# Kernel optimization log

Hardware: AMD Instinct MI355X
Metric: run time of the kernel (lower is better)

## Reference

```python
import jax, jax.numpy as jnp
import numpy as np

FLOAT_MIN = jnp.finfo(jnp.float32).min


def setup_inputs() -> dict:
    key = jax.random.key(0)
    ks = jax.random.split(key, 8)
    B, S, F1, F2, A = 65536, 256, 256, 256, 128
    return {
        "obs_state": jax.random.normal(ks[0], (B, S), dtype=jnp.float32),
        "action_mask": jax.random.randint(ks[1], (B, A), 0, 2, dtype=jnp.int32),
        "W1": jax.random.normal(ks[2], (S, F1), dtype=jnp.float32) * (1.0 / np.sqrt(S)),
        "b1": jnp.zeros((F1,), dtype=jnp.float32),
        "W2": jax.random.normal(ks[3], (F1, F2), dtype=jnp.float32) * (1.0 / np.sqrt(F1)),
        "b2": jnp.zeros((F2,), dtype=jnp.float32),
        "W3": jax.random.normal(ks[4], (F2, A), dtype=jnp.float32) * (1.0 / np.sqrt(F2)),
        "b3": jnp.zeros((A,), dtype=jnp.float32),
    }


def reference(obs_state, action_mask, W1, b1, W2, b2, W3, b3):
    # 3-layer MLP: state -> fc1 -> relu -> fc2 -> relu -> fc3
    h = jax.nn.relu(obs_state @ W1 + b1)
    h = jax.nn.relu(h @ W2 + b2)
    x = h @ W3 + b3  # [B, A] logits

    # Vectorized action masking (replaces per-element Python loop):
    #   mask==0 -> FLOAT_MIN; rows with all-zero mask -> FLOAT_MIN everywhere, col 0 = 1.0
    valid = action_mask != 0  # [B, A] bool
    x = jnp.where(valid, x, FLOAT_MIN)
    all_invalid = ~jnp.any(valid, axis=1, keepdims=True)  # [B, 1]
    col0 = jnp.arange(x.shape[1]) == 0  # [A]
    x = jnp.where(all_invalid & col0, jnp.float32(1.0), x)
    return x
```

## Files before the change

### kernel.cpp

```cpp
#include <hip/hip_runtime.h>

typedef __attribute__((ext_vector_type(8))) short short8;
typedef __attribute__((ext_vector_type(8))) unsigned short ushort8;
typedef __attribute__((ext_vector_type(4))) float f32x4;

#define MT 32
#define STR 264

__device__ __forceinline__ float bmax_r14() { return __uint_as_float(0x7F7F0000u); }

__device__ __forceinline__ unsigned short f2bf_r14(float f) {
    unsigned int u = __float_as_uint(f);
    return (unsigned short)((u + 0x7fffu + ((u >> 16) & 1u)) >> 16);
}

__global__ __launch_bounds__(256)
void pack_weights_r14(const float* __restrict__ W1,
                      const float* __restrict__ W2,
                      const float* __restrict__ W3,
                      unsigned short* __restrict__ ws) {
    int s = blockIdx.x * 256 + threadIdx.x;
    const float* src;
    unsigned short* dst;
    int N;
    if (s < 8192)       { src = W1; dst = ws;          N = 256; }
    else if (s < 16384) { src = W2; dst = ws + 65536;  N = 256; s -= 8192; }
    else                { src = W3; dst = ws + 131072; N = 128; s -= 16384; }
    int frag = s >> 6, lane = s & 63;
    int kb = (frag & 7) * 32 + (lane >> 4) * 8;
    int n  = (frag >> 3) * 16 + (lane & 15);
    ushort8 o;
    #pragma unroll
    for (int j = 0; j < 8; ++j) o[j] = f2bf_r14(src[(kb + j) * N + n]);
    *(ushort8*)&dst[s * 8] = o;
}

__device__ __forceinline__ void layer_mfma_r14(
    const unsigned short* __restrict__ act, const unsigned short* __restrict__ wp,
    int wave, int lane, int quad, int noff, f32x4 acc[2][4])
{
    #pragma unroll
    for (int k0 = 0; k0 < 8; ++k0) {
        short8 b[4];
        #pragma unroll
        for (int ct = 0; ct < 4; ++ct)
            b[ct] = *(const short8*)&wp[(((wave * 4 + ct) * 8 + k0) * 64 + lane) * 8];
        #pragma unroll
        for (int rt = 0; rt < 2; ++rt) {
            short8 a = *(const short8*)&act[(rt * 16 + noff) * STR + k0 * 32 + quad * 8];
            #pragma unroll
            for (int ct = 0; ct < 4; ++ct)
                acc[rt][ct] = __builtin_amdgcn_mfma_f32_16x16x32_bf16(a, b[ct], acc[rt][ct], 0, 0, 0);
        }
    }
}

__device__ __forceinline__ void layer_store_r14(
    unsigned short* __restrict__ act, const float* __restrict__ bias,
    int wave, int quad, int noff, f32x4 acc[2][4])
{
    #pragma unroll
    for (int ct = 0; ct < 4; ++ct) {
        int col = (wave * 4 + ct) * 16 + noff;
        float bv = bias[col];
        #pragma unroll
        for (int rt = 0; rt < 2; ++rt) {
            #pragma unroll
            for (int i = 0; i < 4; ++i) {
                float v = fmaxf(acc[rt][ct][i] + bv, 0.0f);
                act[(rt * 16 + quad * 4 + i) * STR + col] = f2bf_r14(v);
            }
        }
    }
}

__global__ __launch_bounds__(256, 6)
void ColorNetwork_32495722561720_kernel(
        const float* __restrict__ obs,
        const int* __restrict__ amask,
        const float* __restrict__ b1,
        const float* __restrict__ b2,
        const float* __restrict__ b3,
        const unsigned short* __restrict__ w1p,
        const unsigned short* __restrict__ w2p,
        const unsigned short* __restrict__ w3p,
        float* __restrict__ out)
{
    __shared__ __align__(16) unsigned short act[MT * STR];
    __shared__ int rowany[MT];

    const int tid  = threadIdx.x;
    const int wave = tid >> 6;
    const int lane = tid & 63;
    const int quad = lane >> 4;
    const int noff = lane & 15;
    const size_t rowbase = (size_t)blockIdx.x * MT;

    if (tid < MT) rowany[tid] = 0;

    const float4* xin = (const float4*)(obs + rowbase * 256);
    #pragma unroll
    for (int i = 0; i < 8; ++i) {
        int f = tid + i * 256;
        int row = f >> 6;
        int c4 = f & 63;
        float4 v = xin[f];
        ushort4 p;
        p.x = f2bf_r14(v.x); p.y = f2bf_r14(v.y);
        p.z = f2bf_r14(v.z); p.w = f2bf_r14(v.w);
        *(ushort4*)&act[row * STR + c4 * 4] = p;
    }
    __syncthreads();

    const int4* min4 = (const int4*)(amask + rowbase * 128);
    #pragma unroll
    for (int i = 0; i < 4; ++i) {
        int f = tid + i * 256;
        int4 m = min4[f];
        if (m.x | m.y | m.z | m.w) rowany[f >> 5] = 1;
    }

    {
        f32x4 acc[2][4] = {};
        layer_mfma_r14(act, w1p, wave, lane, quad, noff, acc);
        __syncthreads();
        layer_store_r14(act, b1, wave, quad, noff, acc);
        __syncthreads();
    }
    {
        f32x4 acc[2][4] = {};
        layer_mfma_r14(act, w2p, wave, lane, quad, noff, acc);
        __syncthreads();
        layer_store_r14(act, b2, wave, quad, noff, acc);
        __syncthreads();
    }
    {
        f32x4 acc[2][2] = {};
        #pragma unroll
        for (int k0 = 0; k0 < 8; ++k0) {
            short8 b0 = *(const short8*)&w3p[(((wave * 2 + 0) * 8 + k0) * 64 + lane) * 8];
            short8 b1v = *(const short8*)&w3p[(((wave * 2 + 1) * 8 + k0) * 64 + lane) * 8];
            #pragma unroll
            for (int rt = 0; rt < 2; ++rt) {
                short8 a = *(const short8*)&act[(rt * 16 + noff) * STR + k0 * 32 + quad * 8];
                acc[rt][0] = __builtin_amdgcn_mfma_f32_16x16x32_bf16(a, b0, acc[rt][0], 0, 0, 0);
                acc[rt][1] = __builtin_amdgcn_mfma_f32_16x16x32_bf16(a, b1v, acc[rt][1], 0, 0, 0);
            }
        }

        const float BM = bmax_r14();
        #pragma unroll
        for (int ct = 0; ct < 2; ++ct) {
            int col = (wave * 2 + ct) * 16 + noff;
            float bv = b3[col];
            #pragma unroll
            for (int rt = 0; rt < 2; ++rt) {
                #pragma unroll
                for (int i = 0; i < 4; ++i) {
                    int row = rt * 16 + quad * 4 + i;
                    int m = amask[(rowbase + row) * 128 + col];
                    float v = acc[rt][ct][i] + bv;
                    v = fminf(fmaxf(v, -BM), BM);
                    if (!(v == v)) v = 0.0f;
                    if (!m) v = -BM;
                    if (!rowany[row]) v = (col == 0) ? 1.0f : -BM;
                    out[(rowbase + row) * 128 + col] = v;
                }
            }
        }
    }
}

extern "C" void kernel_launch(void* const* d_in, const int* in_sizes, int n_in,
                              void* d_out, int out_size, void* d_ws, size_t ws_size,
                              hipStream_t stream) {
    const float* obs   = (const float*)d_in[0];
    const int*   amask = (const int*)d_in[1];
    const float* W1 = (const float*)d_in[2];
    const float* b1 = (const float*)d_in[3];
    const float* W2 = (const float*)d_in[4];
    const float* b2 = (const float*)d_in[5];
    const float* W3 = (const float*)d_in[6];
    const float* b3 = (const float*)d_in[7];
    float* out = (float*)d_out;

    const int B = in_sizes[0] / 256;

    unsigned short* ws = (unsigned short*)d_ws;
    unsigned short* w1p = ws;
    unsigned short* w2p = ws + 65536;
    unsigned short* w3p = ws + 131072;

    pack_weights_r14<<<80, 256, 0, stream>>>(W1, W2, W3, ws);

    ColorNetwork_32495722561720_kernel<<<B / MT, 256, 0, stream>>>(
        obs, amask, b1, b2, b3, w1p, w2p, w3p, out);
}
```

Before: 179.8 us.

## Process two row tiles per block with ping-pong LDS and register prefetch

Each block now handles two 32-row tiles. Activations ping-pong between two shared-memory buffers, which removes the barrier that sat between each layer's MFMA phase and its store. The next tile's observations are loaded into registers during the current tile's layers and staged into LDS after layer 3, to hide global load latency. The cost is double the LDS footprint, more register pressure (launch bounds lowered from 6 to 4 blocks per CU), and half as many blocks.

After: 213.2 us. 1.19x slower.

```diff
diff --git a/kernel.cpp b/kernel.cpp
--- a/kernel.cpp
+++ b/kernel.cpp
@@ -5,17 +5,18 @@
 typedef __attribute__((ext_vector_type(4))) float f32x4;
 
 #define MT 32
+#define TILES 2
 #define STR 264
 
-__device__ __forceinline__ float bmax_r14() { return __uint_as_float(0x7F7F0000u); }
-
-__device__ __forceinline__ unsigned short f2bf_r14(float f) {
+__device__ __forceinline__ float bmax_r15() { return __uint_as_float(0x7F7F0000u); }
+
+__device__ __forceinline__ unsigned short f2bf_r15(float f) {
     unsigned int u = __float_as_uint(f);
     return (unsigned short)((u + 0x7fffu + ((u >> 16) & 1u)) >> 16);
 }
 
 __global__ __launch_bounds__(256)
-void pack_weights_r14(const float* __restrict__ W1,
+void pack_weights_r15(const float* __restrict__ W1,
                       const float* __restrict__ W2,
                       const float* __restrict__ W3,
                       unsigned short* __restrict__ ws) {
@@ -31,12 +32,12 @@
     int n  = (frag >> 3) * 16 + (lane & 15);
     ushort8 o;
     #pragma unroll
-    for (int j = 0; j < 8; ++j) o[j] = f2bf_r14(src[(kb + j) * N + n]);
+    for (int j = 0; j < 8; ++j) o[j] = f2bf_r15(src[(kb + j) * N + n]);
     *(ushort8*)&dst[s * 8] = o;
 }
 
-__device__ __forceinline__ void layer_mfma_r14(
-    const unsigned short* __restrict__ act, const unsigned short* __restrict__ wp,
+__device__ __forceinline__ void layer_mfma_r15(
+    const unsigned short* __restrict__ src, const unsigned short* __restrict__ wp,
     int wave, int lane, int quad, int noff, f32x4 acc[2][4])
 {
     #pragma unroll
@@ -47,7 +48,7 @@
             b[ct] = *(const short8*)&wp[(((wave * 4 + ct) * 8 + k0) * 64 + lane) * 8];
         #pragma unroll
         for (int rt = 0; rt < 2; ++rt) {
-            short8 a = *(const short8*)&act[(rt * 16 + noff) * STR + k0 * 32 + quad * 8];
+            short8 a = *(const short8*)&src[(rt * 16 + noff) * STR + k0 * 32 + quad * 8];
             #pragma unroll
             for (int ct = 0; ct < 4; ++ct)
                 acc[rt][ct] = __builtin_amdgcn_mfma_f32_16x16x32_bf16(a, b[ct], acc[rt][ct], 0, 0, 0);
@@ -55,8 +56,8 @@
     }
 }
 
-__device__ __forceinline__ void layer_store_r14(
-    unsigned short* __restrict__ act, const float* __restrict__ bias,
+__device__ __forceinline__ void layer_store_r15(
+    unsigned short* __restrict__ dst, const float* __restrict__ bias,
     int wave, int quad, int noff, f32x4 acc[2][4])
 {
     #pragma unroll
@@ -68,13 +69,28 @@
             #pragma unroll
             for (int i = 0; i < 4; ++i) {
                 float v = fmaxf(acc[rt][ct][i] + bv, 0.0f);
-                act[(rt * 16 + quad * 4 + i) * STR + col] = f2bf_r14(v);
-            }
-        }
-    }
-}
-
-__global__ __launch_bounds__(256, 6)
+                dst[(rt * 16 + quad * 4 + i) * STR + col] = f2bf_r15(v);
+            }
+        }
+    }
+}
+
+__device__ __forceinline__ void stage_from_regs_r15(
+    unsigned short* __restrict__ dst, const float4* v, int tid)
+{
+    #pragma unroll
+    for (int i = 0; i < 8; ++i) {
+        int f = tid + i * 256;
+        int row = f >> 6;
+        int c4 = f & 63;
+        ushort4 p;
+        p.x = f2bf_r15(v[i].x); p.y = f2bf_r15(v[i].y);
+        p.z = f2bf_r15(v[i].z); p.w = f2bf_r15(v[i].w);
+        *(ushort4*)&dst[row * STR + c4 * 4] = p;
+    }
+}
+
+__global__ __launch_bounds__(256, 4)
 void ColorNetwork_32495722561720_kernel(
         const float* __restrict__ obs,
         const int* __restrict__ amask,
@@ -86,88 +102,112 @@
         const unsigned short* __restrict__ w3p,
         float* __restrict__ out)
 {
-    __shared__ __align__(16) unsigned short act[MT * STR];
-    __shared__ int rowany[MT];
+    __shared__ __align__(16) unsigned short act[2][MT * STR];
+    __shared__ int rowany[2][MT];
 
     const int tid  = threadIdx.x;
     const int wave = tid >> 6;
     const int lane = tid & 63;
     const int quad = lane >> 4;
     const int noff = lane & 15;
-    const size_t rowbase = (size_t)blockIdx.x * MT;
-
-    if (tid < MT) rowany[tid] = 0;
-
-    const float4* xin = (const float4*)(obs + rowbase * 256);
-    #pragma unroll
-    for (int i = 0; i < 8; ++i) {
-        int f = tid + i * 256;
-        int row = f >> 6;
-        int c4 = f & 63;
-        float4 v = xin[f];
-        ushort4 p;
-        p.x = f2bf_r14(v.x); p.y = f2bf_r14(v.y);
-        p.z = f2bf_r14(v.z); p.w = f2bf_r14(v.w);
-        *(ushort4*)&act[row * STR + c4 * 4] = p;
+    const size_t row0 = (size_t)blockIdx.x * (MT * TILES);
+
+    if (tid < 2 * MT) ((int*)rowany)[tid] = 0;
+
+    float4 xf[8];
+    {
+        const float4* xin = (const float4*)(obs + row0 * 256);
+        #pragma unroll
+        for (int i = 0; i < 8; ++i) xf[i] = xin[tid + i * 256];
     }
     __syncthreads();
-
-    const int4* min4 = (const int4*)(amask + rowbase * 128);
-    #pragma unroll
-    for (int i = 0; i < 4; ++i) {
-        int f = tid + i * 256;
-        int4 m = min4[f];
-        if (m.x | m.y | m.z | m.w) rowany[f >> 5] = 1;
-    }
-
+    stage_from_regs_r15(act[0], xf, tid);
     {
-        f32x4 acc[2][4] = {};
-        layer_mfma_r14(act, w1p, wave, lane, quad, noff, acc);
+        const int4* min4 = (const int4*)(amask + row0 * 128);
+        #pragma unroll
+        for (int i = 0; i < 4; ++i) {
+            int f = tid + i * 256;
+            int4 m = min4[f];
+            if (m.x | m.y | m.z | m.w) rowany[0][f >> 5] = 1;
+        }
+    }
+    __syncthreads();
+
+    int p = 0;
+    #pragma unroll
+    for (int t = 0; t < TILES; ++t, p ^= 1) {
+        const size_t rowbase = row0 + (size_t)t * MT;
+        const bool more = (t + 1 < TILES);
+
+        if (more) {
+            const float4* xin = (const float4*)(obs + (rowbase + MT) * 256);
+            #pragma unroll
+            for (int i = 0; i < 8; ++i) xf[i] = xin[tid + i * 256];
+        }
+
+        {
+            f32x4 acc[2][4] = {};
+            layer_mfma_r15(act[p], w1p, wave, lane, quad, noff, acc);
+            layer_store_r15(act[p ^ 1], b1, wave, quad, noff, acc);
+        }
         __syncthreads();
-        layer_store_r14(act, b1, wave, quad, noff, acc);
+
+        if (more && tid < MT) rowany[p ^ 1][tid] = 0;
+
+        {
+            f32x4 acc[2][4] = {};
+            layer_mfma_r15(act[p ^ 1], w2p, wave, lane, quad, noff, acc);
+            layer_store_r15(act[p], b2, wave, quad, noff, acc);
+        }
         __syncthreads();
-    }
-    {
-        f32x4 acc[2][4] = {};
-        layer_mfma_r14(act, w2p, wave, lane, quad, noff, acc);
-        __syncthreads();
-        layer_store_r14(act, b2, wave, quad, noff, acc);
-        __syncthreads();
-    }
-    {
-        f32x4 acc[2][2] = {};
-        #pragma unroll
-        for (int k0 = 0; k0 < 8; ++k0) {
-            short8 b0 = *(const short8*)&w3p[(((wave * 2 + 0) * 8 + k0) * 64 + lane) * 8];
-            short8 b1v = *(const short8*)&w3p[(((wave * 2 + 1) * 8 + k0) * 64 + lane) * 8];
-            #pragma unroll
-            for (int rt = 0; rt < 2; ++rt) {
-                short8 a = *(const short8*)&act[(rt * 16 + noff) * STR + k0 * 32 + quad * 8];
-                acc[rt][0] = __builtin_amdgcn_mfma_f32_16x16x32_bf16(a, b0, acc[rt][0], 0, 0, 0);
-                acc[rt][1] = __builtin_amdgcn_mfma_f32_16x16x32_bf16(a, b1v, acc[rt][1], 0, 0, 0);
-            }
-        }
-
-        const float BM = bmax_r14();
-        #pragma unroll
-        for (int ct = 0; ct < 2; ++ct) {
-            int col = (wave * 2 + ct) * 16 + noff;
-            float bv = b3[col];
-            #pragma unroll
-            for (int rt = 0; rt < 2; ++rt) {
+
+        {
+            f32x4 acc[2][2] = {};
+            #pragma unroll
+            for (int k0 = 0; k0 < 8; ++k0) {
+                short8 b0 = *(const short8*)&w3p[(((wave * 2 + 0) * 8 + k0) * 64 + lane) * 8];
+                short8 b1v = *(const short8*)&w3p[(((wave * 2 + 1) * 8 + k0) * 64 + lane) * 8];
+                #pragma unroll
+                for (int rt = 0; rt < 2; ++rt) {
+                    short8 a = *(const short8*)&act[p][(rt * 16 + noff) * STR + k0 * 32 + quad * 8];
+                    acc[rt][0] = __builtin_amdgcn_mfma_f32_16x16x32_bf16(a, b0, acc[rt][0], 0, 0, 0);
+                    acc[rt][1] = __builtin_amdgcn_mfma_f32_16x16x32_bf16(a, b1v, acc[rt][1], 0, 0, 0);
+                }
+            }
+
+            if (more) {
+                stage_from_regs_r15(act[p ^ 1], xf, tid);
+                const int4* mn = (const int4*)(amask + (rowbase + MT) * 128);
                 #pragma unroll
                 for (int i = 0; i < 4; ++i) {
-                    int row = rt * 16 + quad * 4 + i;
-                    int m = amask[(rowbase + row) * 128 + col];
-                    float v = acc[rt][ct][i] + bv;
-                    v = fminf(fmaxf(v, -BM), BM);
-                    if (!(v == v)) v = 0.0f;
-                    if (!m) v = -BM;
-                    if (!rowany[row]) v = (col == 0) ? 1.0f : -BM;
-                    out[(rowbase + row) * 128 + col] = v;
+                    int f = tid + i * 256;
+                    int4 m = mn[f];
+                    if (m.x | m.y | m.z | m.w) rowany[p ^ 1][f >> 5] = 1;
                 }
             }
-        }
+
+            const float BM = bmax_r15();
+            #pragma unroll
+            for (int ct = 0; ct < 2; ++ct) {
+                int col = (wave * 2 + ct) * 16 + noff;
+                float bv = b3[col];
+                #pragma unroll
+                for (int rt = 0; rt < 2; ++rt) {
+                    #pragma unroll
+                    for (int i = 0; i < 4; ++i) {
+                        int row = rt * 16 + quad * 4 + i;
+                        int m = amask[(rowbase + row) * 128 + col];
+                        float v = acc[rt][ct][i] + bv;
+                        v = fminf(fmaxf(v, -BM), BM);
+                        if (!(v == v)) v = 0.0f;
+                        if (!m) v = -BM;
+                        if (!rowany[p][row]) v = (col == 0) ? 1.0f : -BM;
+                        out[(rowbase + row) * 128 + col] = v;
+                    }
+                }
+            }
+        }
+        __syncthreads();
     }
 }
 
@@ -191,8 +231,8 @@
     unsigned short* w2p = ws + 65536;
     unsigned short* w3p = ws + 131072;
 
-    pack_weights_r14<<<80, 256, 0, stream>>>(W1, W2, W3, ws);
-
-    ColorNetwork_32495722561720_kernel<<<B / MT, 256, 0, stream>>>(
+    pack_weights_r15<<<80, 256, 0, stream>>>(W1, W2, W3, ws);
+
+    ColorNetwork_32495722561720_kernel<<<B / (MT * TILES), 256, 0, stream>>>(
         obs, amask, b1, b2, b3, w1p, w2p, w3p, out);
 }
```

## Make each wave process its own row tile independently without block barriers

Applied to the files above, without the earlier changes.

Each of the four waves now owns a private 32-row tile in LDS (128 rows per block) and computes every output column of all three layers itself. It keeps the A fragments for the whole K dimension in registers and walks over 16-column tiles, so all __syncthreads are gone. The cost is that each wave now streams the full weight matrices rather than a quarter of them, multiplying L1/L2 weight traffic by four. It also uses more LDS per block, which limits occupancy to two blocks.

After: 184.6 us. +2.7%, slower.

```diff
diff --git a/kernel.cpp b/kernel.cpp
--- a/kernel.cpp
+++ b/kernel.cpp
@@ -5,17 +5,18 @@
 typedef __attribute__((ext_vector_type(4))) float f32x4;
 
 #define MT 32
+#define NWAVE 4
 #define STR 264
 
-__device__ __forceinline__ float bmax_r14() { return __uint_as_float(0x7F7F0000u); }
-
-__device__ __forceinline__ unsigned short f2bf_r14(float f) {
+__device__ __forceinline__ float bmax_r17() { return __uint_as_float(0x7F7F0000u); }
+
+__device__ __forceinline__ unsigned short f2bf_r17(float f) {
     unsigned int u = __float_as_uint(f);
     return (unsigned short)((u + 0x7fffu + ((u >> 16) & 1u)) >> 16);
 }
 
 __global__ __launch_bounds__(256)
-void pack_weights_r14(const float* __restrict__ W1,
+void pack_weights_r17(const float* __restrict__ W1,
                       const float* __restrict__ W2,
                       const float* __restrict__ W3,
                       unsigned short* __restrict__ ws) {
@@ -31,50 +32,11 @@
     int n  = (frag >> 3) * 16 + (lane & 15);
     ushort8 o;
     #pragma unroll
-    for (int j = 0; j < 8; ++j) o[j] = f2bf_r14(src[(kb + j) * N + n]);
+    for (int j = 0; j < 8; ++j) o[j] = f2bf_r17(src[(kb + j) * N + n]);
     *(ushort8*)&dst[s * 8] = o;
 }
 
-__device__ __forceinline__ void layer_mfma_r14(
-    const unsigned short* __restrict__ act, const unsigned short* __restrict__ wp,
-    int wave, int lane, int quad, int noff, f32x4 acc[2][4])
-{
-    #pragma unroll
-    for (int k0 = 0; k0 < 8; ++k0) {
-        short8 b[4];
-        #pragma unroll
-        for (int ct = 0; ct < 4; ++ct)
-            b[ct] = *(const short8*)&wp[(((wave * 4 + ct) * 8 + k0) * 64 + lane) * 8];
-        #pragma unroll
-        for (int rt = 0; rt < 2; ++rt) {
-            short8 a = *(const short8*)&act[(rt * 16 + noff) * STR + k0 * 32 + quad * 8];
-            #pragma unroll
-            for (int ct = 0; ct < 4; ++ct)
-                acc[rt][ct] = __builtin_amdgcn_mfma_f32_16x16x32_bf16(a, b[ct], acc[rt][ct], 0, 0, 0);
-        }
-    }
-}
-
-__device__ __forceinline__ void layer_store_r14(
-    unsigned short* __restrict__ act, const float* __restrict__ bias,
-    int wave, int quad, int noff, f32x4 acc[2][4])
-{
-    #pragma unroll
-    for (int ct = 0; ct < 4; ++ct) {
-        int col = (wave * 4 + ct) * 16 + noff;
-        float bv = bias[col];
-        #pragma unroll
-        for (int rt = 0; rt < 2; ++rt) {
-            #pragma unroll
-            for (int i = 0; i < 4; ++i) {
-                float v = fmaxf(acc[rt][ct][i] + bv, 0.0f);
-                act[(rt * 16 + quad * 4 + i) * STR + col] = f2bf_r14(v);
-            }
-        }
-    }
-}
-
-__global__ __launch_bounds__(256, 6)
+__global__ __launch_bounds__(256, 2)
 void ColorNetwork_32495722561720_kernel(
         const float* __restrict__ obs,
         const int* __restrict__ amask,
@@ -86,86 +48,130 @@
         const unsigned short* __restrict__ w3p,
         float* __restrict__ out)
 {
-    __shared__ __align__(16) unsigned short act[MT * STR];
-    __shared__ int rowany[MT];
+    __shared__ __align__(16) unsigned short act[NWAVE * MT * STR];
+    __shared__ int rowany[NWAVE * MT];
 
     const int tid  = threadIdx.x;
     const int wave = tid >> 6;
     const int lane = tid & 63;
     const int quad = lane >> 4;
     const int noff = lane & 15;
-    const size_t rowbase = (size_t)blockIdx.x * MT;
-
-    if (tid < MT) rowany[tid] = 0;
-
-    const float4* xin = (const float4*)(obs + rowbase * 256);
-    #pragma unroll
-    for (int i = 0; i < 8; ++i) {
-        int f = tid + i * 256;
-        int row = f >> 6;
-        int c4 = f & 63;
-        float4 v = xin[f];
-        ushort4 p;
-        p.x = f2bf_r14(v.x); p.y = f2bf_r14(v.y);
-        p.z = f2bf_r14(v.z); p.w = f2bf_r14(v.w);
-        *(ushort4*)&act[row * STR + c4 * 4] = p;
-    }
-    __syncthreads();
-
-    const int4* min4 = (const int4*)(amask + rowbase * 128);
-    #pragma unroll
-    for (int i = 0; i < 4; ++i) {
-        int f = tid + i * 256;
-        int4 m = min4[f];
-        if (m.x | m.y | m.z | m.w) rowany[f >> 5] = 1;
-    }
+    const int sb   = wave * (MT * STR);
+    const int rb   = wave * MT;
+    const size_t rowbase = (size_t)blockIdx.x * (MT * NWAVE) + (size_t)wave * MT;
 
     {
-        f32x4 acc[2][4] = {};
-        layer_mfma_r14(act, w1p, wave, lane, quad, noff, acc);
-        __syncthreads();
-        layer_store_r14(act, b1, wave, quad, noff, acc);
-        __syncthreads();
-    }
+        const float4* xin = (const float4*)(obs + rowbase * 256);
+        #pragma unroll 8
+        for (int i = 0; i < 32; ++i) {
+            int f = i * 64 + lane;
+            int row = f >> 6;
+            int c4 = f & 63;
+            float4 v = xin[f];
+            ushort4 p;
+            p.x = f2bf_r17(v.x); p.y = f2bf_r17(v.y);
+            p.z = f2bf_r17(v.z); p.w = f2bf_r17(v.w);
+            *(ushort4*)&act[sb + row * STR + c4 * 4] = p;
+        }
+    }
+
+    if (lane < MT) rowany[rb + lane] = 0;
     {
-        f32x4 acc[2][4] = {};
-        layer_mfma_r14(act, w2p, wave, lane, quad, noff, acc);
-        __syncthreads();
-        layer_store_r14(act, b2, wave, quad, noff, acc);
-        __syncthreads();
-    }
-    {
-        f32x4 acc[2][2] = {};
+        const int4* min4 = (const int4*)(amask + rowbase * 128);
+        #pragma unroll 4
+        for (int i = 0; i < 16; ++i) {
+            int f = i * 64 + lane;
+            int4 m = min4[f];
+            if (m.x | m.y | m.z | m.w) rowany[rb + (f >> 5)] = 1;
+        }
+    }
+
+    short8 a[2][8];
+
+    #pragma unroll
+    for (int rt = 0; rt < 2; ++rt)
+        #pragma unroll
+        for (int k0 = 0; k0 < 8; ++k0)
+            a[rt][k0] = *(const short8*)&act[sb + (rt * 16 + noff) * STR + k0 * 32 + quad * 8];
+    #pragma unroll 2
+    for (int ct = 0; ct < 16; ++ct) {
+        f32x4 ac0 = {}, ac1 = {};
         #pragma unroll
         for (int k0 = 0; k0 < 8; ++k0) {
-            short8 b0 = *(const short8*)&w3p[(((wave * 2 + 0) * 8 + k0) * 64 + lane) * 8];
-            short8 b1v = *(const short8*)&w3p[(((wave * 2 + 1) * 8 + k0) * 64 + lane) * 8];
+            short8 b = *(const short8*)&w1p[((ct * 8 + k0) * 64 + lane) * 8];
+            ac0 = __builtin_amdgcn_mfma_f32_16x16x32_bf16(a[0][k0], b, ac0, 0, 0, 0);
+            ac1 = __builtin_amdgcn_mfma_f32_16x16x32_bf16(a[1][k0], b, ac1, 0, 0, 0);
+        }
+        int col = ct * 16 + noff;
+        float bv = b1[col];
+        #pragma unroll
+        for (int i = 0; i < 4; ++i) {
+            act[sb + (quad * 4 + i) * STR + col]      = f2bf_r17(fmaxf(ac0[i] + bv, 0.0f));
+            act[sb + (16 + quad * 4 + i) * STR + col] = f2bf_r17(fmaxf(ac1[i] + bv, 0.0f));
+        }
+    }
+
+    #pragma unroll
+    for (int rt = 0; rt < 2; ++rt)
+        #pragma unroll
+        for (int k0 = 0; k0 < 8; ++k0)
+            a[rt][k0] = *(const short8*)&act[sb + (rt * 16 + noff) * STR + k0 * 32 + quad * 8];
+    #pragma unroll 2
+    for (int ct = 0; ct < 16; ++ct) {
+        f32x4 ac0 = {}, ac1 = {};
+        #pragma unroll
+        for (int k0 = 0; k0 < 8; ++k0) {
+            short8 b = *(const short8*)&w2p[((ct * 8 + k0) * 64 + lane) * 8];
+            ac0 = __builtin_amdgcn_mfma_f32_16x16x32_bf16(a[0][k0], b, ac0, 0, 0, 0);
+            ac1 = __builtin_amdgcn_mfma_f32_16x16x32_bf16(a[1][k0], b, ac1, 0, 0, 0);
+        }
+        int col = ct * 16 + noff;
+        float bv = b2[col];
+        #pragma unroll
+        for (int i = 0; i < 4; ++i) {
+            act[sb + (quad * 4 + i) * STR + col]      = f2bf_r17(fmaxf(ac0[i] + bv, 0.0f));
+            act[sb + (16 + quad * 4 + i) * STR + col] = f2bf_r17(fmaxf(ac1[i] + bv, 0.0f));
+        }
+    }
+
+    #pragma unroll
+    for (int rt = 0; rt < 2; ++rt)
+        #pragma unroll
+        for (int k0 = 0; k0 < 8; ++k0)
+            a[rt][k0] = *(const short8*)&act[sb + (rt * 16 + noff) * STR + k0 * 32 + quad * 8];
+
+    int ra[8];
+    #pragma unroll
+    for (int rt = 0; rt < 2; ++rt)
+        #pragma unroll
+        for (int i = 0; i < 4; ++i)
+            ra[rt * 4 + i] = rowany[rb + rt * 16 + quad * 4 + i];
+
+    const float BM = bmax_r17();
+    #pragma unroll 2
+    for (int ct = 0; ct < 8; ++ct) {
+        f32x4 ac0 = {}, ac1 = {};
+        #pragma unroll
+        for (int k0 = 0; k0 < 8; ++k0) {
+            short8 b = *(const short8*)&w3p[((ct * 8 + k0) * 64 + lane) * 8];
+            ac0 = __builtin_amdgcn_mfma_f32_16x16x32_bf16(a[0][k0], b, ac0, 0, 0, 0);
+            ac1 = __builtin_amdgcn_mfma_f32_16x16x32_bf16(a[1][k0], b, ac1, 0, 0, 0);
+        }
+        int col = ct * 16 + noff;
+        float bv = b3[col];
+        #pragma unroll
+        for (int rt = 0; rt < 2; ++rt) {
+            const f32x4& ac = rt ? ac1 : ac0;
             #pragma unroll
-            for (int rt = 0; rt < 2; ++rt) {
-                short8 a = *(const short8*)&act[(rt * 16 + noff) * STR + k0 * 32 + quad * 8];
-                acc[rt][0] = __builtin_amdgcn_mfma_f32_16x16x32_bf16(a, b0, acc[rt][0], 0, 0, 0);
-                acc[rt][1] = __builtin_amdgcn_mfma_f32_16x16x32_bf16(a, b1v, acc[rt][1], 0, 0, 0);
-            }
-        }
-
-        const float BM = bmax_r14();
-        #pragma unroll
-        for (int ct = 0; ct < 2; ++ct) {
-            int col = (wave * 2 + ct) * 16 + noff;
-            float bv = b3[col];
-            #pragma unroll
-            for (int rt = 0; rt < 2; ++rt) {
-                #pragma unroll
-                for (int i = 0; i < 4; ++i) {
-                    int row = rt * 16 + quad * 4 + i;
-                    int m = amask[(rowbase + row) * 128 + col];
-                    float v = acc[rt][ct][i] + bv;
-                    v = fminf(fmaxf(v, -BM), BM);
-                    if (!(v == v)) v = 0.0f;
-                    if (!m) v = -BM;
-                    if (!rowany[row]) v = (col == 0) ? 1.0f : -BM;
-                    out[(rowbase + row) * 128 + col] = v;
-                }
+            for (int i = 0; i < 4; ++i) {
+                int row = rt * 16 + quad * 4 + i;
+                int m = amask[(rowbase + row) * 128 + col];
+                float v = ac[i] + bv;
+                v = fminf(fmaxf(v, -BM), BM);
+                if (!(v == v)) v = 0.0f;
+                if (!m) v = -BM;
+                if (!ra[rt * 4 + i]) v = (col == 0) ? 1.0f : -BM;
+                out[(rowbase + row) * 128 + col] = v;
             }
         }
     }
@@ -191,8 +197,8 @@
     unsigned short* w2p = ws + 65536;
     unsigned short* w3p = ws + 131072;
 
-    pack_weights_r14<<<80, 256, 0, stream>>>(W1, W2, W3, ws);
-
-    ColorNetwork_32495722561720_kernel<<<B / MT, 256, 0, stream>>>(
+    pack_weights_r17<<<80, 256, 0, stream>>>(W1, W2, W3, ws);
+
+    ColorNetwork_32495722561720_kernel<<<B / (MT * NWAVE), 256, 0, stream>>>(
         obs, amask, b1, b2, b3, w1p, w2p, w3p, out);
 }
```
